# Optimization experiments

Measured on AMD Instinct MI355X. Metric: run time of the kernel, lower is better.

## Reference

```python
import jax, jax.numpy as jnp
import numpy as np

EPS = 1e-6
NUM_HEADS = 16

def _feature_map(x):
    # elu(x) + 1
    return jnp.where(x > 0, x + 1.0, jnp.exp(x))

def setup_inputs() -> dict:
    key = jax.random.key(0)
    ks = jax.random.split(key, 7)
    B, L, S, D = 4, 4096, 4096, 2048
    sc = 1.0 / np.sqrt(D)
    return {
        "query": jax.random.normal(ks[0], (B, L, D), jnp.float32),
        "kv": jax.random.normal(ks[1], (B, S, D), jnp.float32),
        "Wq": jax.random.normal(ks[2], (D, D), jnp.float32) * sc,
        "Wg": jax.random.normal(ks[3], (D, D), jnp.float32) * sc,
        "bg": jnp.ones((D,), jnp.float32),
        "Wkv": jax.random.normal(ks[4], (2 * D, D), jnp.float32) * sc,
        "Wo": jax.random.normal(ks[5], (D, D), jnp.float32) * sc,
    }

def reference(query, kv, Wq, Wg, bg, Wkv, Wo):
    B, L, D = query.shape
    S = kv.shape[1]
    H = NUM_HEADS
    hd = D // H
    q = query @ Wq.T                      # [B,L,D]
    gate = jax.nn.sigmoid(query @ Wg.T + bg)  # [B,L,D]
    kvp = kv @ Wkv.T                      # [B,S,2D]
    k, v = jnp.split(kvp, 2, axis=-1)
    # reshape to heads: [B,H,L,hd]
    q = _feature_map(q.reshape(B, L, H, hd).transpose(0, 2, 1, 3))
    k = _feature_map(k.reshape(B, S, H, hd).transpose(0, 2, 1, 3))
    v = v.reshape(B, S, H, hd).transpose(0, 2, 1, 3)
    kv_summary = jnp.einsum('bhsd,bhse->bhde', k, v)   # [B,H,hd,hd]
    k_sum = k.sum(axis=-2)                              # [B,H,hd]
    z = 1.0 / (jnp.einsum('bhld,bhd->bhl', q, k_sum)[..., None] + EPS)
    attn = jnp.einsum('bhld,bhde->bhle', q, kv_summary) * z  # [B,H,L,hd]
    attn = attn.transpose(0, 2, 1, 3).reshape(B, L, D)
    out = (attn * gate) @ Wo.T
    return out
```

## Files before the change

### kernel.cpp

```cpp
#include <hip/hip_runtime.h>

typedef __attribute__((ext_vector_type(8))) short bf16x8;
typedef __attribute__((ext_vector_type(4))) float f32x4;
typedef __attribute__((ext_vector_type(4))) unsigned int u32x4;

constexpr int L_ = 4096, S_ = 4096, D_ = 2048, H_ = 16, HD_ = 128;
constexpr int LDSS = 72;

__device__ __forceinline__ unsigned short f2bf(float f) {
    unsigned int u = __builtin_bit_cast(unsigned int, f);
    return (unsigned short)((u + 0x7fffu + ((u >> 16) & 1u)) >> 16);
}
__device__ __forceinline__ float bf2f(unsigned short h) {
    unsigned int u = ((unsigned int)h) << 16;
    return __builtin_bit_cast(float, u);
}
__device__ __forceinline__ unsigned long long pack4(float a, float b, float c, float d) {
    return (unsigned long long)f2bf(a) | ((unsigned long long)f2bf(b) << 16)
         | ((unsigned long long)f2bf(c) << 32) | ((unsigned long long)f2bf(d) << 48);
}
__device__ __forceinline__ float featmap(float x) {
    return x > 0.f ? x + 1.f : __expf(x);
}
__device__ __forceinline__ void gload16(const unsigned short* g, unsigned short* l) {
    __builtin_amdgcn_global_load_lds(
        (const __attribute__((address_space(1))) void*)g,
        (__attribute__((address_space(3))) void*)l, 16, 0, 0);
}

__global__ __launch_bounds__(256) void cvt_bf16(
    const float* __restrict__ in, unsigned short* __restrict__ out, int n8)
{
    const int stride = gridDim.x * 256;
    for (int i = blockIdx.x * 256 + threadIdx.x; i < n8; i += stride) {
        const float4 a = ((const float4*)in)[2 * i];
        const float4 b = ((const float4*)in)[2 * i + 1];
        unsigned long long* o = (unsigned long long*)&out[(size_t)i * 8];
        o[0] = pack4(a.x, a.y, a.z, a.w);
        o[1] = pack4(b.x, b.y, b.z, b.w);
    }
}

template<int MODE, int NBN>
__global__ __launch_bounds__(512, 2) void gemm256(
    const unsigned short* __restrict__ A, const unsigned short* __restrict__ B,
    unsigned short* __restrict__ C1, unsigned short* __restrict__ C2,
    float* __restrict__ Cf, const float* __restrict__ bias)
{
    __shared__ alignas(16) unsigned short lds[65536];
    const int tid = threadIdx.x;
    const int lane = tid & 63, w = tid >> 6;
    const int wr = w >> 2, wc = w & 3;
    const int lr = lane & 15;
    const int lk8 = (lane >> 4) * 8;
    const int rsw = (lr & 7) << 3;
    const int lsub = lane >> 3;
    const int scol = ((lane & 7) ^ lsub) * 8;

    const int wg = blockIdx.x;
    const int xcd = wg & 7, u = wg >> 3;
    const int s = u >> 2, q = u & 3;
    const int sbm = s & 3, sbn = s >> 2;
    const int bm = xcd * 8 + sbm * 2 + (q & 1);
    const int bn = sbn * 2 + (q >> 1);
    const int row0 = bm * 256, bcol = bn * 256;

    const unsigned short* Ap = A + (size_t)row0 * D_;
    const unsigned short* Bp = B + (size_t)bcol * D_;
    const int rA = w * 8 + lsub;
    const int rB = ((w * 8 + lsub) >> 5) * 64 + ((w * 8 + lsub) & 31);

    f32x4 acc[8][4] = {};
    bf16x8 av[2][4], bv[2][4];

#define STA(BUF, HH, KT) do { \
    const unsigned short* g_ = Ap + (size_t)((HH) * 64 + rA) * D_ + (KT) * 64 + scol; \
    unsigned short* l_ = &lds[(BUF) * 16384 + (HH) * 8192 + w * 512]; \
    gload16(g_, l_); gload16(g_ + (size_t)128 * D_, l_ + 4096); } while (0)

#define STB(BUF, HH, KT) do { \
    const unsigned short* g_ = Bp + (size_t)(rB + (HH) * 32) * D_ + (KT) * 64 + scol; \
    unsigned short* l_ = &lds[32768 + (BUF) * 16384 + (HH) * 8192 + w * 512]; \
    gload16(g_, l_); gload16(g_ + (size_t)128 * D_, l_ + 4096); } while (0)

#define RD_A(MQ, BUF) \
    _Pragma("unroll") for (int mi = 0; mi < 4; mi++) \
    _Pragma("unroll") for (int ks = 0; ks < 2; ks++) \
        av[ks][mi] = *(const bf16x8*)&lds[(BUF) * 16384 + (MQ) * 8192 \
            + (mi * 16 + lr + wr * 64) * 64 + ((ks * 32 + lk8) ^ rsw)];

#define RD_B(NQ, BUF) \
    _Pragma("unroll") for (int j = 0; j < 2; j++) \
    _Pragma("unroll") for (int ks = 0; ks < 2; ks++) \
        bv[ks][(NQ) * 2 + j] = *(const bf16x8*)&lds[32768 + (BUF) * 16384 + (NQ) * 8192 \
            + (j * 16 + lr + wc * 32) * 64 + ((ks * 32 + lk8) ^ rsw)];

#define MFMA_Q(MQ, NQ) \
    __builtin_amdgcn_s_setprio(1); \
    _Pragma("unroll") for (int mi = 0; mi < 4; mi++) \
    _Pragma("unroll") for (int j = 0; j < 2; j++) \
    _Pragma("unroll") for (int ks = 0; ks < 2; ks++) \
        acc[(MQ) * 4 + mi][(NQ) * 2 + j] = __builtin_amdgcn_mfma_f32_16x16x32_bf16( \
            av[ks][mi], bv[ks][(NQ) * 2 + j], acc[(MQ) * 4 + mi][(NQ) * 2 + j], 0, 0, 0); \
    __builtin_amdgcn_s_setprio(0);

#define BAR __builtin_amdgcn_s_barrier()
#define VM6 asm volatile("s_waitcnt vmcnt(6)" ::: "memory")
#define VM0 asm volatile("s_waitcnt vmcnt(0)" ::: "memory")

    STA(0, 0, 0); STB(0, 0, 0); STB(0, 1, 0); STA(0, 1, 0);
    STA(1, 0, 1); STB(1, 0, 1); STB(1, 1, 1);
    VM6;
    BAR;

    constexpr int NT = D_ / 64;
    for (int i = 0; i < NT / 2 - 1; i++) {
        const int T = 2 * i;
        RD_A(0, 0); RD_B(0, 0); STA(1, 1, T + 1);
        BAR; MFMA_Q(0, 0); BAR;
        RD_B(1, 0); STA(0, 0, T + 2);
        BAR; MFMA_Q(0, 1); BAR;
        RD_A(1, 0); STB(0, 0, T + 2);
        BAR; MFMA_Q(1, 0); BAR;
        STB(0, 1, T + 2);
        VM6; BAR; MFMA_Q(1, 1); BAR;
        RD_A(0, 1); RD_B(0, 1); STA(0, 1, T + 2);
        BAR; MFMA_Q(0, 0); BAR;
        RD_B(1, 1); STA(1, 0, T + 3);
        BAR; MFMA_Q(0, 1); BAR;
        RD_A(1, 1); STB(1, 0, T + 3);
        BAR; MFMA_Q(1, 0); BAR;
        STB(1, 1, T + 3);
        VM6; BAR; MFMA_Q(1, 1); BAR;
    }
    {
        RD_A(0, 0); RD_B(0, 0); STA(1, 1, NT - 1);
        BAR; MFMA_Q(0, 0); BAR;
        RD_B(1, 0);
        BAR; MFMA_Q(0, 1); BAR;
        RD_A(1, 0);
        BAR; MFMA_Q(1, 0); BAR;
        VM0; BAR; MFMA_Q(1, 1); BAR;
        RD_A(0, 1); RD_B(0, 1);
        BAR; MFMA_Q(0, 0); BAR;
        RD_B(1, 1);
        BAR; MFMA_Q(0, 1); BAR;
        RD_A(1, 1);
        BAR; MFMA_Q(1, 0); BAR;
        BAR; MFMA_Q(1, 1); BAR;
    }

    const int rb = (lane >> 4) * 4;
    const bool second = bn >= (NBN / 2);
    if (MODE == 1) {
        unsigned short* TT = lds;
        const int b = row0 >> 12;
        #pragma unroll
        for (int qd = 0; qd < 4; qd++) {
            const int sq = qd >> 1, dh = qd & 1;
            __syncthreads();
            if (wr == sq && (wc >> 1) == dh) {
                #pragma unroll
                for (int m = 0; m < 8; m++) {
                    #pragma unroll
                    for (int n = 0; n < 4; n++) {
                        float x0 = acc[m][n][0], x1 = acc[m][n][1];
                        float x2 = acc[m][n][2], x3 = acc[m][n][3];
                        if (!second) {
                            x0 = featmap(x0); x1 = featmap(x1);
                            x2 = featmap(x2); x3 = featmap(x3);
                        }
                        const int dcol = (wc & 1) * 64 + n * 16 + lr;
                        *(unsigned long long*)&TT[dcol * 136 + m * 16 + rb]
                            = pack4(x0, x1, x2, x3);
                    }
                }
            }
            __syncthreads();
            const int h2 = (bn & 7) * 2 + dh;
            const int s0 = (row0 + sq * 128) & (S_ - 1);
            unsigned short* dst = (second ? C2 : C1) + (size_t)(b * H_ + h2) * HD_ * S_;
            #pragma unroll
            for (int it = 0; it < 4; it++) {
                const int idx = it * 512 + tid;
                const int d = idx >> 4, sc2 = (idx & 15) * 8;
                *(u32x4*)&dst[(size_t)d * S_ + s0 + sc2] = *(const u32x4*)&TT[d * 136 + sc2];
            }
        }
        return;
    }
    #pragma unroll
    for (int m = 0; m < 8; m++) {
        #pragma unroll
        for (int n = 0; n < 4; n++) {
            #pragma unroll
            for (int r = 0; r < 4; r++) {
                const size_t gr = (size_t)(row0 + wr * 128 + m * 16 + rb + r);
                const int gc = bcol + wc * 64 + n * 16 + lr;
                float x = acc[m][n][r];
                if (MODE == 0) {
                    if (!second) {
                        C1[gr * D_ + gc] = f2bf(featmap(x));
                    } else {
                        const int gc2 = gc - D_;
                        float t = x + bias[gc2];
                        C2[gr * D_ + gc2] = f2bf(1.f / (1.f + __expf(-t)));
                    }
                } else {
                    Cf[gr * D_ + gc] = x;
                }
            }
        }
    }
#undef STA
#undef STB
#undef RD_A
#undef RD_B
#undef MFMA_Q
#undef BAR
#undef VM6
#undef VM0
}

__global__ __launch_bounds__(256) void kvsum_part(
    const unsigned short* __restrict__ kT, const unsigned short* __restrict__ vT,
    float* __restrict__ part, float* __restrict__ ksum_part)
{
    __shared__ unsigned short kA[HD_ * LDSS];
    __shared__ unsigned short vB[HD_ * LDSS];
    __shared__ float red[HD_ * 8];
    const int tid = threadIdx.x;
    const int cx = blockIdx.x, bh = blockIdx.y;
    const int lane = tid & 63, w = tid >> 6;
    const int wm = (w >> 1) * 64, wn = (w & 1) * 64;
    const int lr = lane & 15, lk = (lane >> 4) * 8;
    const unsigned short* kb = kT + (size_t)bh * HD_ * S_;
    const unsigned short* vb = vT + (size_t)bh * HD_ * S_;
    f32x4 acc[4][4] = {};
    float ksl[4] = {0.f, 0.f, 0.f, 0.f};
    const int chunk = S_ / 8;
    const int s_begin = cx * chunk;
    for (int s0 = s_begin; s0 < s_begin + chunk; s0 += 64) {
        #pragma unroll
        for (int i = 0; i < 4; i++) {
            int idx = tid + i * 256;
            int d = idx >> 3, sc = (idx & 7) * 8;
            u32x4 kk = *(const u32x4*)&kb[(size_t)d * S_ + s0 + sc];
            *(u32x4*)&kA[d * LDSS + sc] = kk;
            unsigned short t8[8];
            *(u32x4*)t8 = kk;
            float ss = 0.f;
            #pragma unroll
            for (int j = 0; j < 8; j++) ss += bf2f(t8[j]);
            ksl[i] += ss;
            *(u32x4*)&vB[d * LDSS + sc] = *(const u32x4*)&vb[(size_t)d * S_ + s0 + sc];
        }
        __syncthreads();
        #pragma unroll
        for (int ks = 0; ks < 64; ks += 32) {
            bf16x8 av[4], bv[4];
            #pragma unroll
            for (int mi = 0; mi < 4; mi++)
                av[mi] = *(const bf16x8*)&kA[(wm + mi * 16 + lr) * LDSS + ks + lk];
            #pragma unroll
            for (int ni = 0; ni < 4; ni++)
                bv[ni] = *(const bf16x8*)&vB[(wn + ni * 16 + lr) * LDSS + ks + lk];
            #pragma unroll
            for (int mi = 0; mi < 4; mi++)
                #pragma unroll
                for (int ni = 0; ni < 4; ni++)
                    acc[mi][ni] = __builtin_amdgcn_mfma_f32_16x16x32_bf16(
                        av[mi], bv[ni], acc[mi][ni], 0, 0, 0);
        }
        __syncthreads();
    }
    #pragma unroll
    for (int i = 0; i < 4; i++) red[((tid >> 3) + 32 * i) * 8 + (tid & 7)] = ksl[i];
    __syncthreads();
    if (tid < HD_) {
        float s = 0.f;
        #pragma unroll
        for (int j = 0; j < 8; j++) s += red[tid * 8 + j];
        ksum_part[(size_t)cx * (64 * HD_) + bh * HD_ + tid] = s;
    }
    const int rb = (lane >> 4) * 4;
    float* pp = part + ((size_t)cx * 64 + bh) * (HD_ * HD_);
    #pragma unroll
    for (int mi = 0; mi < 4; mi++)
        #pragma unroll
        for (int ni = 0; ni < 4; ni++)
            #pragma unroll
            for (int r = 0; r < 4; r++)
                pp[(wm + mi * 16 + rb + r) * HD_ + wn + ni * 16 + lr] = acc[mi][ni][r];
}

__global__ __launch_bounds__(256) void kvs_reduce(
    const float* __restrict__ part, unsigned short* __restrict__ kvsT,
    const float* __restrict__ ksum_part, float* __restrict__ ksum)
{
    const int idx = blockIdx.x * 256 + threadIdx.x;
    const int e = idx & 127, d2 = (idx >> 7) & 127, bh = idx >> 14;
    float s = 0.f;
    #pragma unroll
    for (int cx = 0; cx < 8; cx++)
        s += part[((size_t)cx * 64 + bh) * 16384 + d2 * 128 + e];
    kvsT[((size_t)bh * 128 + e) * 128 + d2] = f2bf(s);
    if (idx < 64 * 128) {
        float t = 0.f;
        #pragma unroll
        for (int cx = 0; cx < 8; cx++) t += ksum_part[cx * 8192 + idx];
        ksum[idx] = t;
    }
}

__global__ __launch_bounds__(256) void attn_kernel(
    const unsigned short* __restrict__ qf, const unsigned short* __restrict__ kvsT,
    const float* __restrict__ ksum, const unsigned short* __restrict__ gate,
    unsigned short* __restrict__ y)
{
    __shared__ unsigned short qs[128 * 136];
    __shared__ unsigned short bs[128 * LDSS];
    __shared__ float zl[128];
    const int tid = threadIdx.x;
    const int l0 = blockIdx.x * 128;
    const int h = blockIdx.y, b = blockIdx.z;
    const int bh = b * H_ + h;
    const int lane = tid & 63, w = tid >> 6;
    const int wm = (w >> 1) * 64, wn = (w & 1) * 64;
    const int lr = lane & 15, lk = (lane >> 4) * 8;
    const size_t qbase = (size_t)b * L_ * D_ + (size_t)h * HD_;
    #pragma unroll
    for (int i = 0; i < 8; i++) {
        int idx = tid + i * 256;
        int r = idx >> 4, c = (idx & 15) * 8;
        *(u32x4*)&qs[r * 136 + c] = *(const u32x4*)&qf[qbase + (size_t)(l0 + r) * D_ + c];
    }
    __syncthreads();
    if (tid < 128) {
        const float* kp = ksum + bh * HD_;
        float sden = 0.f;
        #pragma unroll 4
        for (int d2 = 0; d2 < HD_; d2++) sden += bf2f(qs[tid * 136 + d2]) * kp[d2];
        zl[tid] = 1.f / (sden + 1e-6f);
    }
    f32x4 acc[4][4] = {};
    for (int kc = 0; kc < 2; kc++) {
        #pragma unroll
        for (int i = 0; i < 4; i++) {
            int idx = tid + i * 256;
            int e = idx >> 3, dc = (idx & 7) * 8;
            *(u32x4*)&bs[e * LDSS + dc] =
                *(const u32x4*)&kvsT[((size_t)bh * 128 + e) * 128 + kc * 64 + dc];
        }
        __syncthreads();
        #pragma unroll
        for (int ks = 0; ks < 64; ks += 32) {
            bf16x8 av[4], bv[4];
            #pragma unroll
            for (int mi = 0; mi < 4; mi++)
                av[mi] = *(const bf16x8*)&qs[(wm + mi * 16 + lr) * 136 + kc * 64 + ks + lk];
            #pragma unroll
            for (int ni = 0; ni < 4; ni++)
                bv[ni] = *(const bf16x8*)&bs[(wn + ni * 16 + lr) * LDSS + ks + lk];
            #pragma unroll
            for (int mi = 0; mi < 4; mi++)
                #pragma unroll
                for (int ni = 0; ni < 4; ni++)
                    acc[mi][ni] = __builtin_amdgcn_mfma_f32_16x16x32_bf16(
                        av[mi], bv[ni], acc[mi][ni], 0, 0, 0);
        }
        __syncthreads();
    }
    const int rb = (lane >> 4) * 4;
    #pragma unroll
    for (int mi = 0; mi < 4; mi++) {
        #pragma unroll
        for (int ni = 0; ni < 4; ni++) {
            #pragma unroll
            for (int r = 0; r < 4; r++) {
                int ll = wm + mi * 16 + rb + r;
                int e = wn + ni * 16 + lr;
                float attn = acc[mi][ni][r] * zl[ll];
                float g = bf2f(gate[qbase + (size_t)(l0 + ll) * D_ + e]);
                y[qbase + (size_t)(l0 + ll) * D_ + e] = f2bf(attn * g);
            }
        }
    }
}

extern "C" void kernel_launch(void* const* d_in, const int* in_sizes, int n_in,
                              void* d_out, int out_size, void* d_ws, size_t ws_size,
                              hipStream_t stream)
{
    (void)in_sizes; (void)n_in; (void)out_size; (void)ws_size;
    const float* query = (const float*)d_in[0];
    const float* kv    = (const float*)d_in[1];
    const float* Wq    = (const float*)d_in[2];
    const float* Wg    = (const float*)d_in[3];
    const float* bg    = (const float*)d_in[4];
    const float* Wkv   = (const float*)d_in[5];
    const float* Wo    = (const float*)d_in[6];
    float* out = (float*)d_out;
    char* ws = (char*)d_ws;

    unsigned short* q_feat = (unsigned short*)(ws);
    unsigned short* gate   = (unsigned short*)(ws + 67108864);
    unsigned short* kTb    = (unsigned short*)(ws + 134217728);
    unsigned short* vTb    = (unsigned short*)(ws + 201326592);
    char* R = ws + 268435456;
    unsigned short* qbf    = (unsigned short*)(R);
    unsigned short* Wqg    = (unsigned short*)(R + 67108864);
    unsigned short* kvbf   = (unsigned short*)(R);
    unsigned short* Wkvb   = (unsigned short*)(R + 67108864);
    float* part            = (float*)(R);
    float* ksum_part       = (float*)(R + 33554432);
    float* ksum            = (float*)(R + 33816576);
    unsigned short* kvsT   = (unsigned short*)(R + 33849344);
    unsigned short* Wob    = (unsigned short*)(R + 83886080);
    unsigned short* ybuf   = kTb;

    dim3 blk(256, 1, 1);
    dim3 blk512(512, 1, 1);
    cvt_bf16<<<dim3(2048), blk, 0, stream>>>(query, qbf, 4194304);
    cvt_bf16<<<dim3(2048), blk, 0, stream>>>(Wq, Wqg, 524288);
    cvt_bf16<<<dim3(2048), blk, 0, stream>>>(Wg, Wqg + 4194304, 524288);
    cvt_bf16<<<dim3(2048), blk, 0, stream>>>(Wo, Wob, 524288);
    gemm256<0, 16><<<dim3(1024), blk512, 0, stream>>>(qbf, Wqg, q_feat, gate, nullptr, bg);
    cvt_bf16<<<dim3(2048), blk, 0, stream>>>(kv, kvbf, 4194304);
    cvt_bf16<<<dim3(2048), blk, 0, stream>>>(Wkv, Wkvb, 1048576);
    gemm256<1, 16><<<dim3(1024), blk512, 0, stream>>>(kvbf, Wkvb, kTb, vTb, nullptr, nullptr);
    kvsum_part<<<dim3(8, 64), blk, 0, stream>>>(kTb, vTb, part, ksum_part);
    kvs_reduce<<<dim3(4096), blk, 0, stream>>>(part, kvsT, ksum_part, ksum);
    attn_kernel<<<dim3(32, 16, 4), blk, 0, stream>>>(q_feat, kvsT, ksum, gate, ybuf);
    gemm256<2, 8><<<dim3(512), blk512, 0, stream>>>(ybuf, Wob, nullptr, nullptr, out, nullptr);
}
```

Measured before the change: 961.7 us.

## Restructure GEMM main loop to prefetch B fragments and halve barriers

Reorders the GEMM main loop so the B-operand LDS fragments for the next half-tile are read right after the previous MFMA quadrant, before the barrier. Each stage now uses one barrier (plus a sched_barrier) instead of two. The MFMA quadrant order changes to (0,0),(0,1),(1,1),(1,0) so B fragments can be reused across adjacent quadrants. The aim is to cut barrier stalls and hide LDS read latency behind MFMA work. In exchange there is more register pressure and a tighter ordering requirement between LDS reads and overwrites of the buffers being staged.

```diff
diff --git a/kernel.cpp b/kernel.cpp
--- a/kernel.cpp
+++ b/kernel.cpp
@@ -104,6 +104,7 @@
             av[ks][mi], bv[ks][(NQ) * 2 + j], acc[(MQ) * 4 + mi][(NQ) * 2 + j], 0, 0, 0); \
     __builtin_amdgcn_s_setprio(0);
 
+#define SB0 __builtin_amdgcn_sched_barrier(0)
 #define BAR __builtin_amdgcn_s_barrier()
 #define VM6 asm volatile("s_waitcnt vmcnt(6)" ::: "memory")
 #define VM0 asm volatile("s_waitcnt vmcnt(0)" ::: "memory")
@@ -112,42 +113,47 @@
     STA(1, 0, 1); STB(1, 0, 1); STB(1, 1, 1);
     VM6;
     BAR;
+    RD_B(0, 0); RD_B(1, 0);
 
     constexpr int NT = D_ / 64;
     for (int i = 0; i < NT / 2 - 1; i++) {
         const int T = 2 * i;
-        RD_A(0, 0); RD_B(0, 0); STA(1, 1, T + 1);
-        BAR; MFMA_Q(0, 0); BAR;
-        RD_B(1, 0); STA(0, 0, T + 2);
-        BAR; MFMA_Q(0, 1); BAR;
+        RD_A(0, 0); STA(1, 1, T + 1);
+        MFMA_Q(0, 0); SB0; BAR;
+        STA(0, 0, T + 2);
+        MFMA_Q(0, 1); SB0; BAR;
         RD_A(1, 0); STB(0, 0, T + 2);
-        BAR; MFMA_Q(1, 0); BAR;
+        MFMA_Q(1, 1); SB0; BAR;
         STB(0, 1, T + 2);
-        VM6; BAR; MFMA_Q(1, 1); BAR;
-        RD_A(0, 1); RD_B(0, 1); STA(0, 1, T + 2);
-        BAR; MFMA_Q(0, 0); BAR;
-        RD_B(1, 1); STA(1, 0, T + 3);
-        BAR; MFMA_Q(0, 1); BAR;
+        MFMA_Q(1, 0);
+        VM6; RD_B(0, 1); RD_B(1, 1);
+        SB0; BAR;
+        RD_A(0, 1); STA(0, 1, T + 2);
+        MFMA_Q(0, 0); SB0; BAR;
+        STA(1, 0, T + 3);
+        MFMA_Q(0, 1); SB0; BAR;
         RD_A(1, 1); STB(1, 0, T + 3);
-        BAR; MFMA_Q(1, 0); BAR;
+        MFMA_Q(1, 1); SB0; BAR;
         STB(1, 1, T + 3);
-        VM6; BAR; MFMA_Q(1, 1); BAR;
+        MFMA_Q(1, 0);
+        VM6; RD_B(0, 0); RD_B(1, 0);
+        SB0; BAR;
     }
     {
-        RD_A(0, 0); RD_B(0, 0); STA(1, 1, NT - 1);
-        BAR; MFMA_Q(0, 0); BAR;
-        RD_B(1, 0);
-        BAR; MFMA_Q(0, 1); BAR;
+        RD_A(0, 0); STA(1, 1, NT - 1);
+        MFMA_Q(0, 0); SB0; BAR;
+        MFMA_Q(0, 1); SB0; BAR;
         RD_A(1, 0);
-        BAR; MFMA_Q(1, 0); BAR;
-        VM0; BAR; MFMA_Q(1, 1); BAR;
-        RD_A(0, 1); RD_B(0, 1);
-        BAR; MFMA_Q(0, 0); BAR;
-        RD_B(1, 1);
-        BAR; MFMA_Q(0, 1); BAR;
+        MFMA_Q(1, 1); SB0; BAR;
+        MFMA_Q(1, 0);
+        VM0; RD_B(0, 1); RD_B(1, 1);
+        SB0; BAR;
+        RD_A(0, 1);
+        MFMA_Q(0, 0); SB0; BAR;
+        MFMA_Q(0, 1); SB0; BAR;
         RD_A(1, 1);
-        BAR; MFMA_Q(1, 0); BAR;
-        BAR; MFMA_Q(1, 1); BAR;
+        MFMA_Q(1, 1); SB0; BAR;
+        MFMA_Q(1, 0); SB0; BAR;
     }
 
     const int rb = (lane >> 4) * 4;
@@ -217,6 +223,7 @@
 #undef RD_A
 #undef RD_B
 #undef MFMA_Q
+#undef SB0
 #undef BAR
 #undef VM6
 #undef VM0
```

Result: no change. 951.0 us (-1.1%).
